# Optimization experiments

Hardware: AMD Instinct MI355X
Metric: run time of the kernel (lower is better)

## Reference

```python
import jax, jax.numpy as jnp
import numpy as np

L, H, FG, C = 2, 4, 8, 2            # n_layer, grid_heads, grid_feats, grid_channels
HNODE, HNET, HPIN = 96, 32, 16      # hidden node/net/pin feats
ONODE, ONET, NT = 32, 32, 4         # out node/net feats, n_target


def _leaky(x, s=0.01):
    return jnp.where(x >= 0, x, s * x)


def _edge_softmax(e, dst, n):
    # e: [E,H] scores, softmax over incoming edges per dst node
    m = jax.ops.segment_max(e, dst, num_segments=n)
    m = jnp.where(jnp.isfinite(m), m, 0.0)
    ex = jnp.exp(e - m[dst])
    s = jax.ops.segment_sum(ex, dst, num_segments=n)
    return ex / jnp.maximum(s[dst], 1e-9)


def _gat(x, src, dst, fc_w, attn_l, attn_r, bias, n):
    # DGL GATConv: fc (no bias), additive attention, leaky_relu(0.2), edge softmax, sum, +bias
    h = (x @ fc_w).reshape(n, H, FG)                      # [N,H,F]
    el = jnp.sum(h * attn_l, -1)                          # [N,H]
    er = jnp.sum(h * attn_r, -1)
    e = _leaky(el[src] + er[dst], 0.2)                    # [E,H]
    a = _edge_softmax(e, dst, n)
    out = jax.ops.segment_sum(h[src] * a[..., None], dst, num_segments=n)
    return out + bias.reshape(1, H, FG)                   # [N,H,F]


def _graphconv(x, src, dst, w, b, n_src, n_dst):
    # DGL GraphConv norm='both': D_src^-1/2 (xW) aggregated, D_dst^-1/2, + bias
    deg_out = jnp.maximum(jax.ops.segment_sum(jnp.ones(src.shape, jnp.float32), src, num_segments=n_src), 1.0)
    deg_in = jnp.maximum(jax.ops.segment_sum(jnp.ones(dst.shape, jnp.float32), dst, num_segments=n_dst), 1.0)
    h = (x * deg_out[:, None] ** -0.5) @ w
    agg = jax.ops.segment_sum(h[src], dst, num_segments=n_dst)
    return agg * deg_in[:, None] ** -0.5 + b


def _nnconv(x_src, src, dst, efeat, lin2_w, lin2_b, b, n_dst):
    # DGL NNConv (aggregator='mean'): per-edge weight matrix from edge_func=lin2
    W = (efeat @ lin2_w + lin2_b).reshape(-1, HNET, ONODE)   # [E,in,out]
    msg = jnp.einsum('ei,eio->eo', x_src[src], W)            # [E,out]
    deg = jnp.maximum(jax.ops.segment_sum(jnp.ones(dst.shape, jnp.float32), dst, num_segments=n_dst), 1.0)
    agg = jax.ops.segment_sum(msg, dst, num_segments=n_dst) / deg[:, None]
    return agg + b


def setup_inputs() -> dict:
    key = jax.random.key(0)
    ks = jax.random.split(key, 32)
    Nn, Nnet, Ep, Eg = 50000, 50000, 150000, 400000
    IN_NODE, IN_NET, IN_PIN = 16, 8, 8

    def rn(k, shape, scale=0.1):
        return jax.random.normal(k, shape, jnp.float32) * scale

    return {
        'in_node_feat': rn(ks[0], (Nn, IN_NODE), 1.0),
        'in_net_feat': rn(ks[1], (Nnet, IN_NET), 1.0),
        'in_pin_feat': rn(ks[2], (Ep, IN_PIN), 1.0),
        'node_lin_w': rn(ks[3], (IN_NODE, HNODE)), 'node_lin_b': rn(ks[4], (HNODE,)),
        'net_lin_w': rn(ks[5], (IN_NET, HNET)), 'net_lin_b': rn(ks[6], (HNET,)),
        'pin_lin_w': rn(ks[7], (IN_PIN, HPIN)), 'pin_lin_b': rn(ks[8], (HPIN,)),
        'gat_fc_w': rn(ks[9], (L, HNODE, H * FG)),
        'gat_attn_l': rn(ks[10], (L, H, FG)), 'gat_attn_r': rn(ks[11], (L, H, FG)),
        'gat_bias': rn(ks[12], (L, H * FG)),
        'gconv_w': rn(ks[13], (L, HNODE, ONET)), 'gconv_b': rn(ks[14], (L, ONET)),
        'lin2_w': rn(ks[15], (L, HPIN, HNET * ONODE)), 'lin2_b': rn(ks[16], (L, HNET * ONODE)),
        'nnconv_b': rn(ks[17], (L, ONODE)),
        'out1_w': rn(ks[18], (IN_NODE + HNODE, HNODE)), 'out1_b': rn(ks[19], (HNODE,)),
        'out2_w': rn(ks[20], (HNODE, HNODE)), 'out2_b': rn(ks[21], (HNODE,)),
        'out3_w': rn(ks[22], (HNODE, NT)), 'out3_b': rn(ks[23], (NT,)),
        'pins_src': jax.random.randint(ks[24], (Ep,), 0, Nn),
        'pins_dst': jax.random.randint(ks[25], (Ep,), 0, Nnet),
        'grid_src': jax.random.randint(ks[26], (C, Eg), 0, Nn),
        'grid_dst': jax.random.randint(ks[27], (C, Eg), 0, Nn),
    }


def reference(in_node_feat, in_net_feat, in_pin_feat, node_lin_w, node_lin_b,
              net_lin_w, net_lin_b, pin_lin_w, pin_lin_b, gat_fc_w, gat_attn_l,
              gat_attn_r, gat_bias, gconv_w, gconv_b, lin2_w, lin2_b, nnconv_b,
              out1_w, out1_b, out2_w, out2_b, out3_w, out3_b,
              pins_src, pins_dst, grid_src, grid_dst):
    Nn = in_node_feat.shape[0]
    Nnet = in_net_feat.shape[0]
    node = _leaky(in_node_feat @ node_lin_w + node_lin_b)
    net = _leaky(in_net_feat @ net_lin_w + net_lin_b)
    pin = _leaky(in_pin_feat @ pin_lin_w + pin_lin_b)
    for i in range(L):
        grids = [_gat(node, grid_src[j], grid_dst[j], gat_fc_w[i], gat_attn_l[i],
                      gat_attn_r[i], gat_bias[i], Nn) for j in range(C)]
        grid_out = jnp.concatenate(grids, -1).reshape(Nn, -1)   # [N, H*C*FG]
        # 'pins': node -> net (GraphConv); 'pinned': net -> node (NNConv, reversed pin edges)
        net_out = _graphconv(node, pins_src, pins_dst, gconv_w[i], gconv_b[i], Nn, Nnet)
        node_out = _nnconv(net, pins_dst, pins_src, pin, lin2_w[i], lin2_b[i], nnconv_b[i], Nn)
        node = jnp.tanh(jnp.concatenate([grid_out, node_out], -1))
        net = jnp.tanh(net_out)
    h = jnp.tanh(jnp.concatenate([in_node_feat, node], -1) @ out1_w + out1_b)
    h = jnp.tanh(h @ out2_w + out2_b)
    return jax.nn.sigmoid(h @ out3_w + out3_b)
```

## Files before the change

### kernel.cpp

```cpp
#include <hip/hip_runtime.h>
#include <math.h>


#define CAPG 48
#define CAPP 24
#define GB_U16 64
#define PD_U16 32
#define PS_STRIDE 64

typedef unsigned short ushort_t;
typedef unsigned int uint_t;
typedef __attribute__((ext_vector_type(8))) short bf16x8;
typedef __attribute__((ext_vector_type(4))) float f32x4;

static __device__ __forceinline__ float bf2f(ushort_t u) {
    return __uint_as_float(((unsigned)u) << 16);
}
static __device__ __forceinline__ ushort_t f2bf(float f) {
    unsigned i = __float_as_uint(f);
    unsigned r = (i + 0x7FFFu + ((i >> 16) & 1u)) >> 16;
    return (ushort_t)r;
}
static __device__ __forceinline__ uint_t pk2(float a, float b) {
    return (uint_t)f2bf(a) | ((uint_t)f2bf(b) << 16);
}
static __device__ __forceinline__ float lo2(uint_t u) { return __uint_as_float(u << 16); }
static __device__ __forceinline__ float hi2(uint_t u) { return __uint_as_float(u & 0xFFFF0000u); }

template <int ACT, int K1, int K2, int M, int R, bool OUT16>
__global__ void gemm_tiled(const float* __restrict__ X1,
                           const float* __restrict__ X2,
                           const float* __restrict__ rowscale,
                           const float* __restrict__ W,
                           const float* __restrict__ bias,
                           void* __restrict__ Yv, int N) {
    constexpr int K = K1 + K2;
    constexpr int MG = M / 4;
    constexpr int RG = 256 / MG;
    __shared__ float sW[K * M];
    for (int t = threadIdx.x; t < K * M; t += 256) sW[t] = W[t];
    __syncthreads();
    const float4* sW4 = (const float4*)sW;
    const int lane = threadIdx.x % MG;
    const int rsub = threadIdx.x / MG;
    if (rsub >= RG) return;
    const long long bstride = (long long)gridDim.x * RG * R;
    for (long long base = (long long)blockIdx.x * RG * R + rsub; base < N; base += bstride) {
        long long rows[R];
        bool ok[R];
        float4 acc[R];
#pragma unroll
        for (int j = 0; j < R; ++j) {
            rows[j] = base + (long long)j * RG;
            ok[j] = rows[j] < N;
            if (!ok[j]) rows[j] = base;
            acc[j] = {0.f, 0.f, 0.f, 0.f};
        }
        {
            const float4* x4[R];
#pragma unroll
            for (int j = 0; j < R; ++j) x4[j] = (const float4*)(X1 + rows[j] * K1);
#pragma unroll 2
            for (int k4 = 0; k4 < K1 / 4; ++k4) {
                float4 w0 = sW4[(k4 * 4 + 0) * MG + lane];
                float4 w1 = sW4[(k4 * 4 + 1) * MG + lane];
                float4 w2 = sW4[(k4 * 4 + 2) * MG + lane];
                float4 w3 = sW4[(k4 * 4 + 3) * MG + lane];
#pragma unroll
                for (int j = 0; j < R; ++j) {
                    float4 xv = x4[j][k4];
                    acc[j].x += xv.x * w0.x + xv.y * w1.x + xv.z * w2.x + xv.w * w3.x;
                    acc[j].y += xv.x * w0.y + xv.y * w1.y + xv.z * w2.y + xv.w * w3.y;
                    acc[j].z += xv.x * w0.z + xv.y * w1.z + xv.z * w2.z + xv.w * w3.z;
                    acc[j].w += xv.x * w0.w + xv.y * w1.w + xv.z * w2.w + xv.w * w3.w;
                }
            }
        }
        if (K2 > 0) {
            const float4* x4[R];
#pragma unroll
            for (int j = 0; j < R; ++j) x4[j] = (const float4*)(X2 + rows[j] * K2);
#pragma unroll 2
            for (int k4 = 0; k4 < K2 / 4; ++k4) {
                float4 w0 = sW4[(K1 + k4 * 4 + 0) * MG + lane];
                float4 w1 = sW4[(K1 + k4 * 4 + 1) * MG + lane];
                float4 w2 = sW4[(K1 + k4 * 4 + 2) * MG + lane];
                float4 w3 = sW4[(K1 + k4 * 4 + 3) * MG + lane];
#pragma unroll
                for (int j = 0; j < R; ++j) {
                    float4 xv = x4[j][k4];
                    acc[j].x += xv.x * w0.x + xv.y * w1.x + xv.z * w2.x + xv.w * w3.x;
                    acc[j].y += xv.x * w0.y + xv.y * w1.y + xv.z * w2.y + xv.w * w3.y;
                    acc[j].z += xv.x * w0.z + xv.y * w1.z + xv.z * w2.z + xv.w * w3.z;
                    acc[j].w += xv.x * w0.w + xv.y * w1.w + xv.z * w2.w + xv.w * w3.w;
                }
            }
        }
#pragma unroll
        for (int j = 0; j < R; ++j) {
            if (!ok[j]) continue;
            float4 a = acc[j];
            if (rowscale) {
                float rs = rowscale[rows[j]];
                a.x *= rs; a.y *= rs; a.z *= rs; a.w *= rs;
            }
            if (bias) {
                float4 bv = *(const float4*)(bias + lane * 4);
                a.x += bv.x; a.y += bv.y; a.z += bv.z; a.w += bv.w;
            }
            if (ACT == 1) {
                a.x = a.x >= 0.f ? a.x : 0.01f * a.x;
                a.y = a.y >= 0.f ? a.y : 0.01f * a.y;
                a.z = a.z >= 0.f ? a.z : 0.01f * a.z;
                a.w = a.w >= 0.f ? a.w : 0.01f * a.w;
            } else if (ACT == 2) {
                a.x = tanhf(a.x); a.y = tanhf(a.y);
                a.z = tanhf(a.z); a.w = tanhf(a.w);
            } else if (ACT == 3) {
                a.x = 1.f / (1.f + expf(-a.x)); a.y = 1.f / (1.f + expf(-a.y));
                a.z = 1.f / (1.f + expf(-a.z)); a.w = 1.f / (1.f + expf(-a.w));
            }
            if (OUT16) {
                uint2 v;
                v.x = pk2(a.x, a.y);
                v.y = pk2(a.z, a.w);
                *(uint2*)((ushort_t*)Yv + rows[j] * M + lane * 4) = v;
            } else {
                *(float4*)((float*)Yv + rows[j] * M + lane * 4) = a;
            }
        }
    }
}

__global__ void gemm_dual32(const float* __restrict__ X,
                            const float* __restrict__ rsN,
                            const float* __restrict__ W1,
                            const float* __restrict__ W2,
                            ushort_t* __restrict__ Y1, ushort_t* __restrict__ Y2, int N) {
    __shared__ float sW1[96 * 32];
    __shared__ float sW2[96 * 32];
    for (int t = threadIdx.x; t < 96 * 32; t += 256) {
        sW1[t] = W1[t];
        sW2[t] = W2[t];
    }
    __syncthreads();
    const float4* sW1_4 = (const float4*)sW1;
    const float4* sW2_4 = (const float4*)sW2;
    const int lane = threadIdx.x & 7;
    const int rsub = threadIdx.x >> 3;
    long long n0 = (long long)blockIdx.x * 64 + rsub;
    long long n1 = n0 + 32;
    if (n0 >= N) return;
    bool ok1 = n1 < N;
    const float4* x0 = (const float4*)(X + n0 * 96);
    const float4* x1 = (const float4*)(X + (ok1 ? n1 : n0) * 96);
    float4 a0 = {0.f, 0.f, 0.f, 0.f}, b0 = a0, a1 = a0, b1 = a0;
#pragma unroll 2
    for (int k4 = 0; k4 < 24; ++k4) {
        float4 xv0 = x0[k4];
        float4 xv1 = x1[k4];
#pragma unroll
        for (int kk = 0; kk < 4; ++kk) {
            float4 w1v = sW1_4[(k4 * 4 + kk) * 8 + lane];
            float4 w2v = sW2_4[(k4 * 4 + kk) * 8 + lane];
            float xs0 = kk == 0 ? xv0.x : kk == 1 ? xv0.y : kk == 2 ? xv0.z : xv0.w;
            float xs1 = kk == 0 ? xv1.x : kk == 1 ? xv1.y : kk == 2 ? xv1.z : xv1.w;
            a0.x += xs0 * w1v.x; a0.y += xs0 * w1v.y; a0.z += xs0 * w1v.z; a0.w += xs0 * w1v.w;
            b0.x += xs0 * w2v.x; b0.y += xs0 * w2v.y; b0.z += xs0 * w2v.z; b0.w += xs0 * w2v.w;
            a1.x += xs1 * w1v.x; a1.y += xs1 * w1v.y; a1.z += xs1 * w1v.z; a1.w += xs1 * w1v.w;
            b1.x += xs1 * w2v.x; b1.y += xs1 * w2v.y; b1.z += xs1 * w2v.z; b1.w += xs1 * w2v.w;
        }
    }
    {
        float rs = rsN[n0];
        uint2 va = {pk2(a0.x, a0.y), pk2(a0.z, a0.w)};
        uint2 vb = {pk2(b0.x * rs, b0.y * rs), pk2(b0.z * rs, b0.w * rs)};
        *(uint2*)(Y1 + n0 * 32 + lane * 4) = va;
        *(uint2*)(Y2 + n0 * 32 + lane * 4) = vb;
    }
    if (ok1) {
        float rs = rsN[n1];
        uint2 va = {pk2(a1.x, a1.y), pk2(a1.z, a1.w)};
        uint2 vb = {pk2(b1.x * rs, b1.y * rs), pk2(b1.z * rs, b1.w * rs)};
        *(uint2*)(Y1 + n1 * 32 + lane * 4) = va;
        *(uint2*)(Y2 + n1 * 32 + lane * 4) = vb;
    }
}

__global__ void zero_counts(ushort_t* __restrict__ gB0, ushort_t* __restrict__ gB1,
                            ushort_t* __restrict__ pdB, int* __restrict__ psB,
                            int Nn, int Nnet) {
    int i = blockIdx.x * blockDim.x + threadIdx.x;
    int mx = Nn > Nnet ? Nn : Nnet;
    for (; i < mx; i += gridDim.x * blockDim.x) {
        if (i < Nn) {
            *(int*)(gB0 + (long long)i * GB_U16) = 0;
            *(int*)(gB1 + (long long)i * GB_U16) = 0;
            psB[(long long)i * PS_STRIDE] = 0;
        }
        if (i < Nnet) *(int*)(pdB + (long long)i * PD_U16) = 0;
    }
}

__global__ void csr_build(const int* __restrict__ ps, const int* __restrict__ pd,
                          const int* __restrict__ gs0, const int* __restrict__ gd0,
                          const int* __restrict__ gs1, const int* __restrict__ gd1,
                          ushort_t* __restrict__ gB0, ushort_t* __restrict__ gB1,
                          ushort_t* __restrict__ pdB, int* __restrict__ psB,
                          int Ep, int Eg) {
    int total = 2 * Ep + 2 * Eg;
    for (int t = blockIdx.x * blockDim.x + threadIdx.x; t < total; t += gridDim.x * blockDim.x) {
        if (t < Ep) {
            int s = ps[t];
            int* b = psB + (long long)s * PS_STRIDE;
            int r = atomicAdd(b, 1);
            if (r < CAPP) ((int2*)b)[1 + r] = make_int2(t, pd[t]);
        } else if (t < 2 * Ep) {
            int e = t - Ep;
            int d = pd[e];
            ushort_t* b = pdB + (long long)d * PD_U16;
            int r = atomicAdd((int*)b, 1);
            if (r < CAPP) b[2 + r] = (ushort_t)ps[e];
        } else if (t < 2 * Ep + Eg) {
            int e = t - 2 * Ep;
            int d = gd0[e];
            ushort_t* b = gB0 + (long long)d * GB_U16;
            int r = atomicAdd((int*)b, 1);
            if (r < CAPG) b[2 + r] = (ushort_t)gs0[e];
        } else {
            int e = t - 2 * Ep - Eg;
            int d = gd1[e];
            ushort_t* b = gB1 + (long long)d * GB_U16;
            int r = atomicAdd((int*)b, 1);
            if (r < CAPG) b[2 + r] = (ushort_t)gs1[e];
        }
    }
}

__global__ void deg_xform2(const int* __restrict__ psB, const ushort_t* __restrict__ pdB,
                           float* __restrict__ rs, float* __restrict__ inv,
                           float* __restrict__ rsNet, int Nn, int Nnet) {
    int i = blockIdx.x * blockDim.x + threadIdx.x;
    int mx = Nn > Nnet ? Nn : Nnet;
    for (; i < mx; i += gridDim.x * blockDim.x) {
        if (i < Nn) {
            float d = fmaxf((float)psB[(long long)i * PS_STRIDE], 1.f);
            rs[i] = 1.f / sqrtf(d);
            inv[i] = 1.f / d;
        }
        if (i < Nnet) {
            float d = fmaxf((float)*(const int*)(pdB + (long long)i * PD_U16), 1.f);
            rsNet[i] = 1.f / sqrtf(d);
        }
    }
}

__global__ void gat_scores(const ushort_t* __restrict__ h, const float* __restrict__ al,
                           const float* __restrict__ ar, float* __restrict__ el,
                           float* __restrict__ er, int N) {
    int idx = blockIdx.x * blockDim.x + threadIdx.x;
    if (idx >= N * 4) return;
    int n = idx >> 2, hd = idx & 3;
    uint4 hv = *(const uint4*)(h + (long long)n * 32 + hd * 8);
    float f0 = lo2(hv.x), f1 = hi2(hv.x), f2 = lo2(hv.y), f3 = hi2(hv.y);
    float f4 = lo2(hv.z), f5 = hi2(hv.z), f6 = lo2(hv.w), f7 = hi2(hv.w);
    const float* a = al + hd * 8;
    const float* r = ar + hd * 8;
    float sl = f0 * a[0] + f1 * a[1] + f2 * a[2] + f3 * a[3] +
               f4 * a[4] + f5 * a[5] + f6 * a[6] + f7 * a[7];
    float sr = f0 * r[0] + f1 * r[1] + f2 * r[2] + f3 * r[3] +
               f4 * r[4] + f5 * r[5] + f6 * r[6] + f7 * r[7];
    el[idx] = sl;
    er[idx] = sr;
}

__global__ void gat_gather8(const ushort_t* __restrict__ gB0, const ushort_t* __restrict__ gB1,
                            const float* __restrict__ el, const float* __restrict__ er,
                            const ushort_t* __restrict__ gh, const float* __restrict__ gbias,
                            float* __restrict__ out, int N) {
    int idx = blockIdx.x * blockDim.x + threadIdx.x;
    if (idx >= N * 8) return;
    int d = idx >> 3;
    int rem = idx & 7;
    int hd = rem >> 1;
    int ch = rem & 1;
    float rd = er[d * 4 + hd];
    const ushort_t* b = (ch ? gB1 : gB0) + (long long)d * GB_U16;
    int c = *(const int*)b;
    c = c < CAPG ? c : CAPG;
    float sum = 0.f;
    float acc0 = 0.f, acc1 = 0.f, acc2 = 0.f, acc3 = 0.f;
    float acc4 = 0.f, acc5 = 0.f, acc6 = 0.f, acc7 = 0.f;
    for (int p = 0; p < c; ++p) {
        int s = b[2 + p];
        float v = el[s * 4 + hd] + rd;
        v = v >= 0.f ? v : 0.2f * v;
        float w = __expf(v);
        uint4 hv = *(const uint4*)(gh + (long long)s * 32 + hd * 8);
        sum += w;
        acc0 += w * lo2(hv.x); acc1 += w * hi2(hv.x);
        acc2 += w * lo2(hv.y); acc3 += w * hi2(hv.y);
        acc4 += w * lo2(hv.z); acc5 += w * hi2(hv.z);
        acc6 += w * lo2(hv.w); acc7 += w * hi2(hv.w);
    }
    float inv = 1.f / fmaxf(sum, 1e-9f);
    const float4* gb4 = (const float4*)(gbias + hd * 8);
    float4 b0 = gb4[0], b1 = gb4[1];
    float* op = out + (long long)d * 96 + hd * 16 + ch * 8;
    float4 r0, r1;
    r0.x = tanhf(acc0 * inv + b0.x); r0.y = tanhf(acc1 * inv + b0.y);
    r0.z = tanhf(acc2 * inv + b0.z); r0.w = tanhf(acc3 * inv + b0.w);
    r1.x = tanhf(acc4 * inv + b1.x); r1.y = tanhf(acc5 * inv + b1.y);
    r1.z = tanhf(acc6 * inv + b1.z); r1.w = tanhf(acc7 * inv + b1.w);
    *(float4*)(op) = r0;
    *(float4*)(op + 4) = r1;
}

__global__ void gconv_gather(const ushort_t* __restrict__ pdB, const ushort_t* __restrict__ h,
                             const float* __restrict__ rsNet, const float* __restrict__ gb,
                             ushort_t* __restrict__ out, int N) {
    long long total = (long long)N * 32;
    long long stride = (long long)gridDim.x * blockDim.x;
    for (long long idx = (long long)blockIdx.x * blockDim.x + threadIdx.x; idx < total; idx += stride) {
        int n = (int)(idx >> 5), c = (int)(idx & 31);
        const ushort_t* b = pdB + (long long)n * PD_U16;
        int cn = *(const int*)b;
        cn = cn < CAPP ? cn : CAPP;
        float acc = 0.f;
        for (int p = 0; p < cn; ++p) acc += bf2f(h[(long long)b[2 + p] * 32 + c]);
        out[idx] = f2bf(tanhf(acc * rsNet[n] + gb[c]));
    }
}

__global__ void nn_accum(const int* __restrict__ psB, const float* __restrict__ pinf,
                         const ushort_t* __restrict__ net, ushort_t* __restrict__ G, int N) {
    int t = blockIdx.x * blockDim.x + threadIdx.x;
    int n = t >> 5, i = t & 31;
    if (n >= N) return;
    const int* b = psB + (long long)n * PS_STRIDE;
    int cn = b[0]; cn = cn < CAPP ? cn : CAPP;
    const int2* ed2 = (const int2*)b + 1;
    float g[17];
#pragma unroll
    for (int k = 0; k < 17; ++k) g[k] = 0.f;
    for (int p = 0; p < cn; ++p) {
        int2 ed = ed2[p];
        float nv = bf2f(net[(long long)ed.y * 32 + i]);
        const float4* pr4 = (const float4*)(pinf + (long long)ed.x * 16);
        float4 a0 = pr4[0], a1 = pr4[1], a2 = pr4[2], a3 = pr4[3];
        g[0] += a0.x * nv;  g[1] += a0.y * nv;  g[2] += a0.z * nv;  g[3] += a0.w * nv;
        g[4] += a1.x * nv;  g[5] += a1.y * nv;  g[6] += a1.z * nv;  g[7] += a1.w * nv;
        g[8] += a2.x * nv;  g[9] += a2.y * nv;  g[10] += a2.z * nv; g[11] += a2.w * nv;
        g[12] += a3.x * nv; g[13] += a3.y * nv; g[14] += a3.z * nv; g[15] += a3.w * nv;
        g[16] += nv;
    }
    ushort_t* Gp = G + (long long)n * 544 + i;
#pragma unroll
    for (int k = 0; k < 17; ++k) Gp[k * 32] = f2bf(g[k]);
}

__launch_bounds__(256, 4)
__global__ void nn_gemm_mfma(const ushort_t* __restrict__ G,
                             const float* __restrict__ w,
                             const float* __restrict__ b2,
                             const float* __restrict__ invN,
                             const float* __restrict__ nnb,
                             float* __restrict__ out, int N) {
    __shared__ ushort_t sB[2 * 17 * 64 * 8];
    for (int idx = threadIdx.x; idx < 2 * 17 * 64 * 8; idx += 256) {
        int e = idx & 7;
        int l = (idx >> 3) & 63;
        int rest = idx >> 9;
        int s = rest % 17;
        int t = rest / 17;
        int grow = s * 32 + ((l >> 4) << 3) + e;
        int col = t * 16 + (l & 15);
        float v = (grow < 512) ? w[grow * 32 + col] : b2[(grow - 512) * 32 + col];
        sB[idx] = f2bf(v);
    }
    __syncthreads();
    const int lane = threadIdx.x & 63;
    const int wv = threadIdx.x >> 6;
    long long rowBase = (long long)blockIdx.x * 64 + (long long)wv * 16;
    if (rowBase >= N) return;
    const int r15 = lane & 15;
    const int kgrp = lane >> 4;
    long long arow = rowBase + r15;
    if (arow >= N) arow = N - 1;
    const ushort_t* gp = G + arow * 544 + kgrp * 8;
    f32x4 acc0 = {0.f, 0.f, 0.f, 0.f};
    f32x4 acc1 = {0.f, 0.f, 0.f, 0.f};
#pragma unroll
    for (int s = 0; s < 17; ++s) {
        bf16x8 a = *(const bf16x8*)(gp + s * 32);
        bf16x8 bb0 = *(const bf16x8*)(sB + ((0 * 17 + s) * 64 + lane) * 8);
        bf16x8 bb1 = *(const bf16x8*)(sB + ((1 * 17 + s) * 64 + lane) * 8);
        acc0 = __builtin_amdgcn_mfma_f32_16x16x32_bf16(a, bb0, acc0, 0, 0, 0);
        acc1 = __builtin_amdgcn_mfma_f32_16x16x32_bf16(a, bb1, acc1, 0, 0, 0);
    }
#pragma unroll
    for (int r = 0; r < 4; ++r) {
        long long row = rowBase + kgrp * 4 + r;
        if (row < N) {
            float iv = invN[row];
            float* op = out + row * 96 + 64;
            op[r15] = tanhf(acc0[r] * iv + nnb[r15]);
            op[16 + r15] = tanhf(acc1[r] * iv + nnb[16 + r15]);
        }
    }
}

__launch_bounds__(256, 4)
__global__ void mlp1_mfma(const float* __restrict__ X1, const float* __restrict__ X2,
                          const float* __restrict__ W, const float* __restrict__ bias,
                          ushort_t* __restrict__ Y, int N) {
    __shared__ ushort_t sB[6 * 4 * 64 * 8];
    for (int idx = threadIdx.x; idx < 6 * 4 * 64 * 8; idx += 256) {
        int e = idx & 7;
        int l = (idx >> 3) & 63;
        int rest = idx >> 9;
        int s = rest & 3;
        int t = rest >> 2;
        int grow = s * 32 + ((l >> 4) << 3) + e;
        int col = t * 16 + (l & 15);
        float v = (grow < 112) ? W[grow * 96 + col] : 0.f;
        sB[idx] = f2bf(v);
    }
    __syncthreads();
    const int lane = threadIdx.x & 63;
    const int wv = threadIdx.x >> 6;
    long long rowBase = (long long)blockIdx.x * 64 + (long long)wv * 16;
    if (rowBase >= N) return;
    const int r15 = lane & 15;
    const int kgrp = lane >> 4;
    long long arow = rowBase + r15;
    if (arow >= N) arow = N - 1;
    bf16x8 a[4];
#pragma unroll
    for (int s = 0; s < 4; ++s) {
        int k0 = s * 32 + kgrp * 8;
        float f[8];
        if (k0 < 16) {
            const float4* p = (const float4*)(X1 + arow * 16 + k0);
            float4 u = p[0], v = p[1];
            f[0] = u.x; f[1] = u.y; f[2] = u.z; f[3] = u.w;
            f[4] = v.x; f[5] = v.y; f[6] = v.z; f[7] = v.w;
        } else if (k0 < 112) {
            const float4* p = (const float4*)(X2 + arow * 96 + (k0 - 16));
            float4 u = p[0], v = p[1];
            f[0] = u.x; f[1] = u.y; f[2] = u.z; f[3] = u.w;
            f[4] = v.x; f[5] = v.y; f[6] = v.z; f[7] = v.w;
        } else {
#pragma unroll
            for (int j = 0; j < 8; ++j) f[j] = 0.f;
        }
        bf16x8 av;
#pragma unroll
        for (int j = 0; j < 8; ++j) av[j] = (short)f2bf(f[j]);
        a[s] = av;
    }
    f32x4 acc[6];
#pragma unroll
    for (int t = 0; t < 6; ++t) acc[t] = {0.f, 0.f, 0.f, 0.f};
#pragma unroll
    for (int s = 0; s < 4; ++s) {
#pragma unroll
        for (int t = 0; t < 6; ++t) {
            bf16x8 bb = *(const bf16x8*)(sB + ((t * 4 + s) * 64 + lane) * 8);
            acc[t] = __builtin_amdgcn_mfma_f32_16x16x32_bf16(a[s], bb, acc[t], 0, 0, 0);
        }
    }
#pragma unroll
    for (int r = 0; r < 4; ++r) {
        long long row = rowBase + kgrp * 4 + r;
        if (row < N) {
            ushort_t* op = Y + row * 96;
#pragma unroll
            for (int t = 0; t < 6; ++t) {
                int col = t * 16 + r15;
                op[col] = f2bf(tanhf(acc[t][r] + bias[col]));
            }
        }
    }
}

__launch_bounds__(256, 4)
__global__ void mlp2_mfma(const ushort_t* __restrict__ X,
                          const float* __restrict__ W, const float* __restrict__ bias,
                          float* __restrict__ Y, int N) {
    __shared__ ushort_t sB[6 * 3 * 64 * 8];
    for (int idx = threadIdx.x; idx < 6 * 3 * 64 * 8; idx += 256) {
        int e = idx & 7;
        int l = (idx >> 3) & 63;
        int rest = idx >> 9;
        int s = rest % 3;
        int t = rest / 3;
        int grow = s * 32 + ((l >> 4) << 3) + e;
        int col = t * 16 + (l & 15);
        sB[idx] = f2bf(W[grow * 96 + col]);
    }
    __syncthreads();
    const int lane = threadIdx.x & 63;
    const int wv = threadIdx.x >> 6;
    long long rowBase = (long long)blockIdx.x * 64 + (long long)wv * 16;
    if (rowBase >= N) return;
    const int r15 = lane & 15;
    const int kgrp = lane >> 4;
    long long arow = rowBase + r15;
    if (arow >= N) arow = N - 1;
    const ushort_t* xp = X + arow * 96 + kgrp * 8;
    f32x4 acc[6];
#pragma unroll
    for (int t = 0; t < 6; ++t) acc[t] = {0.f, 0.f, 0.f, 0.f};
#pragma unroll
    for (int s = 0; s < 3; ++s) {
        bf16x8 a = *(const bf16x8*)(xp + s * 32);
#pragma unroll
        for (int t = 0; t < 6; ++t) {
            bf16x8 bb = *(const bf16x8*)(sB + ((t * 3 + s) * 64 + lane) * 8);
            acc[t] = __builtin_amdgcn_mfma_f32_16x16x32_bf16(a, bb, acc[t], 0, 0, 0);
        }
    }
#pragma unroll
    for (int r = 0; r < 4; ++r) {
        long long row = rowBase + kgrp * 4 + r;
        if (row < N) {
            float* op = Y + row * 96;
#pragma unroll
            for (int t = 0; t < 6; ++t) {
                int col = t * 16 + r15;
                op[col] = tanhf(acc[t][r] + bias[col]);
            }
        }
    }
}

extern "C" void kernel_launch(void* const* d_in, const int* in_sizes, int n_in,
                              void* d_out, int out_size, void* d_ws, size_t ws_size,
                              hipStream_t stream) {
    const float* in_node = (const float*)d_in[0];
    const float* in_net = (const float*)d_in[1];
    const float* in_pinf = (const float*)d_in[2];
    const float* node_lin_w = (const float*)d_in[3];
    const float* node_lin_b = (const float*)d_in[4];
    const float* net_lin_w = (const float*)d_in[5];
    const float* net_lin_b = (const float*)d_in[6];
    const float* pin_lin_w = (const float*)d_in[7];
    const float* pin_lin_b = (const float*)d_in[8];
    const float* gat_fc_w = (const float*)d_in[9];
    const float* gat_attn_l = (const float*)d_in[10];
    const float* gat_attn_r = (const float*)d_in[11];
    const float* gat_bias = (const float*)d_in[12];
    const float* gconv_w = (const float*)d_in[13];
    const float* gconv_b = (const float*)d_in[14];
    const float* lin2_w = (const float*)d_in[15];
    const float* lin2_b = (const float*)d_in[16];
    const float* nnconv_bias = (const float*)d_in[17];
    const float* out1_w = (const float*)d_in[18];
    const float* out1_b = (const float*)d_in[19];
    const float* out2_w = (const float*)d_in[20];
    const float* out2_b = (const float*)d_in[21];
    const float* out3_w = (const float*)d_in[22];
    const float* out3_b = (const float*)d_in[23];
    const int* pins_src = (const int*)d_in[24];
    const int* pins_dst = (const int*)d_in[25];
    const int* grid_src = (const int*)d_in[26];
    const int* grid_dst = (const int*)d_in[27];

    const int Nn = in_sizes[0] / 16;
    const int Nnet = in_sizes[1] / 8;
    const int Ep = in_sizes[2] / 8;
    const int Eg = in_sizes[26] / 2;

    char* base = (char*)d_ws;
    size_t off = 0;
    auto alloc = [&](size_t bytes) -> void* {
        void* p = base + off;
        off += (bytes + 255) & ~(size_t)255;
        return p;
    };
    float* pin = (float*)alloc((size_t)Ep * 16 * 4);
    ushort_t* G = (ushort_t*)alloc((size_t)Nn * 544 * 2);
    float* rsN = (float*)alloc((size_t)Nn * 4);
    float* invN = (float*)alloc((size_t)Nn * 4);
    float* rsNet = (float*)alloc((size_t)Nnet * 4);
    ushort_t* gridB0 = (ushort_t*)alloc((size_t)Nn * GB_U16 * 2);
    ushort_t* gridB1 = (ushort_t*)alloc((size_t)Nn * GB_U16 * 2);
    ushort_t* pinDstB = (ushort_t*)alloc((size_t)Nnet * PD_U16 * 2);
    int* pinSrcB = (int*)alloc((size_t)Nn * PS_STRIDE * 4);
    float* nodeA = (float*)alloc((size_t)Nn * 96 * 4);
    float* nodeB = (float*)alloc((size_t)Nn * 96 * 4);
    ushort_t* netA = (ushort_t*)alloc((size_t)Nnet * 32 * 2);
    ushort_t* netB = (ushort_t*)alloc((size_t)Nnet * 32 * 2);
    ushort_t* gat_h = (ushort_t*)alloc((size_t)Nn * 32 * 2);
    float* el = (float*)alloc((size_t)Nn * 4 * 4);
    float* er = (float*)alloc((size_t)Nn * 4 * 4);
    ushort_t* gconv_h = (ushort_t*)alloc((size_t)Nn * 32 * 2);
    ushort_t* h1 = (ushort_t*)alloc((size_t)Nn * 96 * 2);

    auto gsz = [](long long total) -> int {
        long long b = (total + 255) / 256;
        if (b < 1) b = 1;
        if (b > 4096) b = 4096;
        return (int)b;
    };

    const int maxN = Nn > Nnet ? Nn : Nnet;
    const long long scatterT = 2LL * Ep + 2LL * Eg;

    zero_counts<<<gsz(maxN), 256, 0, stream>>>(gridB0, gridB1, pinDstB, pinSrcB, Nn, Nnet);
    csr_build<<<gsz(scatterT), 256, 0, stream>>>(pins_src, pins_dst,
                                                 grid_src, grid_dst, grid_src + Eg, grid_dst + Eg,
                                                 gridB0, gridB1, pinDstB, pinSrcB, Ep, Eg);
    deg_xform2<<<gsz(maxN), 256, 0, stream>>>(pinSrcB, pinDstB, rsN, invN, rsNet, Nn, Nnet);

    auto blocks_for = [](long long N, int M, int R) -> int {
        int rowsPerBlock = (256 / (M / 4)) * R;
        long long b = (N + rowsPerBlock - 1) / rowsPerBlock;
        if (b > 2048) b = 2048;
        if (b < 1) b = 1;
        return (int)b;
    };

    gemm_tiled<1, 16, 0, 96, 4, false><<<blocks_for(Nn, 96, 4), 256, 0, stream>>>(
        in_node, nullptr, nullptr, node_lin_w, node_lin_b, nodeA, Nn);
    gemm_tiled<1, 8, 0, 32, 2, true><<<blocks_for(Nnet, 32, 2), 256, 0, stream>>>(
        in_net, nullptr, nullptr, net_lin_w, net_lin_b, netA, Nnet);
    gemm_tiled<1, 8, 0, 16, 2, false><<<blocks_for(Ep, 16, 2), 256, 0, stream>>>(
        in_pinf, nullptr, nullptr, pin_lin_w, pin_lin_b, pin, Ep);

    float* node_cur = nodeA; float* node_nxt = nodeB;
    ushort_t* net_cur = netA; ushort_t* net_nxt = netB;

    for (int i = 0; i < 2; ++i) {
        gemm_dual32<<<(Nn + 63) / 64, 256, 0, stream>>>(
            node_cur, rsN, gat_fc_w + (size_t)i * 96 * 32, gconv_w + (size_t)i * 96 * 32,
            gat_h, gconv_h, Nn);
        gat_scores<<<(Nn * 4 + 255) / 256, 256, 0, stream>>>(
            gat_h, gat_attn_l + i * 32, gat_attn_r + i * 32, el, er, Nn);

        gat_gather8<<<(Nn * 8 + 255) / 256, 256, 0, stream>>>(
            gridB0, gridB1, el, er, gat_h, gat_bias + i * 32, node_nxt, Nn);

        gconv_gather<<<gsz((long long)Nnet * 32), 256, 0, stream>>>(
            pinDstB, gconv_h, rsNet, gconv_b + i * 32, net_nxt, Nnet);

        nn_accum<<<(Nn * 32 + 255) / 256, 256, 0, stream>>>(
            pinSrcB, pin, net_cur, G, Nn);
        nn_gemm_mfma<<<(Nn + 63) / 64, 256, 0, stream>>>(
            G, lin2_w + (size_t)i * 16 * 1024, lin2_b + (size_t)i * 1024,
            invN, nnconv_bias + i * 32, node_nxt, Nn);

        float* t = node_cur; node_cur = node_nxt; node_nxt = t;
        ushort_t* u = net_cur; net_cur = net_nxt; net_nxt = u;
    }

    mlp1_mfma<<<(Nn + 63) / 64, 256, 0, stream>>>(
        in_node, node_cur, out1_w, out1_b, h1, Nn);
    float* h2 = node_nxt;
    mlp2_mfma<<<(Nn + 63) / 64, 256, 0, stream>>>(
        h1, out2_w, out2_b, h2, Nn);
    gemm_tiled<3, 96, 0, 4, 1, false><<<blocks_for(Nn, 4, 1), 256, 0, stream>>>(
        h2, nullptr, nullptr, out3_w, out3_b, (float*)d_out, Nn);
}
```

Baseline: 345.6 us.

## Fuse NNConv edge accumulation with MFMA GEMM via shared memory; store pin feats bf16

Merges the per-node accumulation kernel and the MFMA GEMM into one kernel that builds the 16x544 G tile in LDS and multiplies it by lin2 weights there, so the large G intermediate never goes to global memory. Pin features are now stored as bf16, which halves their gather traffic. In exchange, each 512-thread block rebuilds the 17KB weight tile for only 16 rows, and only one wave does the MFMA while the other seven sit idle. LDS use per block also grows, which lowers occupancy.

```diff
diff --git a/kernel.cpp b/kernel.cpp
--- a/kernel.cpp
+++ b/kernel.cpp
@@ -332,42 +332,15 @@
     }
 }
 
-__global__ void nn_accum(const int* __restrict__ psB, const float* __restrict__ pinf,
-                         const ushort_t* __restrict__ net, ushort_t* __restrict__ G, int N) {
-    int t = blockIdx.x * blockDim.x + threadIdx.x;
-    int n = t >> 5, i = t & 31;
-    if (n >= N) return;
-    const int* b = psB + (long long)n * PS_STRIDE;
-    int cn = b[0]; cn = cn < CAPP ? cn : CAPP;
-    const int2* ed2 = (const int2*)b + 1;
-    float g[17];
-#pragma unroll
-    for (int k = 0; k < 17; ++k) g[k] = 0.f;
-    for (int p = 0; p < cn; ++p) {
-        int2 ed = ed2[p];
-        float nv = bf2f(net[(long long)ed.y * 32 + i]);
-        const float4* pr4 = (const float4*)(pinf + (long long)ed.x * 16);
-        float4 a0 = pr4[0], a1 = pr4[1], a2 = pr4[2], a3 = pr4[3];
-        g[0] += a0.x * nv;  g[1] += a0.y * nv;  g[2] += a0.z * nv;  g[3] += a0.w * nv;
-        g[4] += a1.x * nv;  g[5] += a1.y * nv;  g[6] += a1.z * nv;  g[7] += a1.w * nv;
-        g[8] += a2.x * nv;  g[9] += a2.y * nv;  g[10] += a2.z * nv; g[11] += a2.w * nv;
-        g[12] += a3.x * nv; g[13] += a3.y * nv; g[14] += a3.z * nv; g[15] += a3.w * nv;
-        g[16] += nv;
-    }
-    ushort_t* Gp = G + (long long)n * 544 + i;
-#pragma unroll
-    for (int k = 0; k < 17; ++k) Gp[k * 32] = f2bf(g[k]);
-}
-
-__launch_bounds__(256, 4)
-__global__ void nn_gemm_mfma(const ushort_t* __restrict__ G,
-                             const float* __restrict__ w,
-                             const float* __restrict__ b2,
-                             const float* __restrict__ invN,
-                             const float* __restrict__ nnb,
-                             float* __restrict__ out, int N) {
+__launch_bounds__(512, 1)
+__global__ void nn_fused(const int* __restrict__ psB, const ushort_t* __restrict__ pinf,
+                         const ushort_t* __restrict__ net,
+                         const float* __restrict__ w, const float* __restrict__ b2,
+                         const float* __restrict__ invN, const float* __restrict__ nnb,
+                         float* __restrict__ out, int N) {
+    __shared__ ushort_t sG[16 * 544];
     __shared__ ushort_t sB[2 * 17 * 64 * 8];
-    for (int idx = threadIdx.x; idx < 2 * 17 * 64 * 8; idx += 256) {
+    for (int idx = threadIdx.x; idx < 2 * 17 * 64 * 8; idx += 512) {
         int e = idx & 7;
         int l = (idx >> 3) & 63;
         int rest = idx >> 9;
@@ -378,34 +351,60 @@
         float v = (grow < 512) ? w[grow * 32 + col] : b2[(grow - 512) * 32 + col];
         sB[idx] = f2bf(v);
     }
+    const int n_local = threadIdx.x >> 5;
+    const int i = threadIdx.x & 31;
+    long long n = (long long)blockIdx.x * 16 + n_local;
+    float g[17];
+#pragma unroll
+    for (int k = 0; k < 17; ++k) g[k] = 0.f;
+    if (n < N) {
+        const int* b = psB + n * PS_STRIDE;
+        int cn = b[0]; cn = cn < CAPP ? cn : CAPP;
+        const int2* ed2 = (const int2*)b + 1;
+        for (int p = 0; p < cn; ++p) {
+            int2 ed = ed2[p];
+            float nv = bf2f(net[(long long)ed.y * 32 + i]);
+            const uint4* pr = (const uint4*)(pinf + (long long)ed.x * 16);
+            uint4 u0 = pr[0], u1 = pr[1];
+            g[0] += lo2(u0.x) * nv;  g[1] += hi2(u0.x) * nv;
+            g[2] += lo2(u0.y) * nv;  g[3] += hi2(u0.y) * nv;
+            g[4] += lo2(u0.z) * nv;  g[5] += hi2(u0.z) * nv;
+            g[6] += lo2(u0.w) * nv;  g[7] += hi2(u0.w) * nv;
+            g[8] += lo2(u1.x) * nv;  g[9] += hi2(u1.x) * nv;
+            g[10] += lo2(u1.y) * nv; g[11] += hi2(u1.y) * nv;
+            g[12] += lo2(u1.z) * nv; g[13] += hi2(u1.z) * nv;
+            g[14] += lo2(u1.w) * nv; g[15] += hi2(u1.w) * nv;
+            g[16] += nv;
+        }
+    }
+    ushort_t* gp = sG + n_local * 544 + i;
+#pragma unroll
+    for (int k = 0; k < 17; ++k) gp[k * 32] = f2bf(g[k]);
     __syncthreads();
-    const int lane = threadIdx.x & 63;
-    const int wv = threadIdx.x >> 6;
-    long long rowBase = (long long)blockIdx.x * 64 + (long long)wv * 16;
-    if (rowBase >= N) return;
-    const int r15 = lane & 15;
-    const int kgrp = lane >> 4;
-    long long arow = rowBase + r15;
-    if (arow >= N) arow = N - 1;
-    const ushort_t* gp = G + arow * 544 + kgrp * 8;
-    f32x4 acc0 = {0.f, 0.f, 0.f, 0.f};
-    f32x4 acc1 = {0.f, 0.f, 0.f, 0.f};
-#pragma unroll
-    for (int s = 0; s < 17; ++s) {
-        bf16x8 a = *(const bf16x8*)(gp + s * 32);
-        bf16x8 bb0 = *(const bf16x8*)(sB + ((0 * 17 + s) * 64 + lane) * 8);
-        bf16x8 bb1 = *(const bf16x8*)(sB + ((1 * 17 + s) * 64 + lane) * 8);
-        acc0 = __builtin_amdgcn_mfma_f32_16x16x32_bf16(a, bb0, acc0, 0, 0, 0);
-        acc1 = __builtin_amdgcn_mfma_f32_16x16x32_bf16(a, bb1, acc1, 0, 0, 0);
-    }
-#pragma unroll
-    for (int r = 0; r < 4; ++r) {
-        long long row = rowBase + kgrp * 4 + r;
-        if (row < N) {
-            float iv = invN[row];
-            float* op = out + row * 96 + 64;
-            op[r15] = tanhf(acc0[r] * iv + nnb[r15]);
-            op[16 + r15] = tanhf(acc1[r] * iv + nnb[16 + r15]);
+    if (threadIdx.x < 64) {
+        const int lane = threadIdx.x;
+        const int r15 = lane & 15;
+        const int kgrp = lane >> 4;
+        const ushort_t* ap = sG + r15 * 544 + kgrp * 8;
+        f32x4 acc0 = {0.f, 0.f, 0.f, 0.f};
+        f32x4 acc1 = {0.f, 0.f, 0.f, 0.f};
+#pragma unroll
+        for (int s = 0; s < 17; ++s) {
+            bf16x8 a = *(const bf16x8*)(ap + s * 32);
+            bf16x8 bb0 = *(const bf16x8*)(sB + ((0 * 17 + s) * 64 + lane) * 8);
+            bf16x8 bb1 = *(const bf16x8*)(sB + ((1 * 17 + s) * 64 + lane) * 8);
+            acc0 = __builtin_amdgcn_mfma_f32_16x16x32_bf16(a, bb0, acc0, 0, 0, 0);
+            acc1 = __builtin_amdgcn_mfma_f32_16x16x32_bf16(a, bb1, acc1, 0, 0, 0);
+        }
+#pragma unroll
+        for (int r = 0; r < 4; ++r) {
+            long long row = (long long)blockIdx.x * 16 + kgrp * 4 + r;
+            if (row < N) {
+                float iv = invN[row];
+                float* op = out + row * 96 + 64;
+                op[r15] = tanhf(acc0[r] * iv + nnb[r15]);
+                op[16 + r15] = tanhf(acc1[r] * iv + nnb[16 + r15]);
+            }
         }
     }
 }
@@ -579,8 +578,7 @@
         off += (bytes + 255) & ~(size_t)255;
         return p;
     };
-    float* pin = (float*)alloc((size_t)Ep * 16 * 4);
-    ushort_t* G = (ushort_t*)alloc((size_t)Nn * 544 * 2);
+    ushort_t* pin = (ushort_t*)alloc((size_t)Ep * 16 * 2);
     float* rsN = (float*)alloc((size_t)Nn * 4);
     float* invN = (float*)alloc((size_t)Nn * 4);
     float* rsNet = (float*)alloc((size_t)Nnet * 4);
@@ -626,7 +624,7 @@
         in_node, nullptr, nullptr, node_lin_w, node_lin_b, nodeA, Nn);
     gemm_tiled<1, 8, 0, 32, 2, true><<<blocks_for(Nnet, 32, 2), 256, 0, stream>>>(
         in_net, nullptr, nullptr, net_lin_w, net_lin_b, netA, Nnet);
-    gemm_tiled<1, 8, 0, 16, 2, false><<<blocks_for(Ep, 16, 2), 256, 0, stream>>>(
+    gemm_tiled<1, 8, 0, 16, 2, true><<<blocks_for(Ep, 16, 2), 256, 0, stream>>>(
         in_pinf, nullptr, nullptr, pin_lin_w, pin_lin_b, pin, Ep);
 
     float* node_cur = nodeA; float* node_nxt = nodeB;
@@ -645,11 +643,9 @@
         gconv_gather<<<gsz((long long)Nnet * 32), 256, 0, stream>>>(
             pinDstB, gconv_h, rsNet, gconv_b + i * 32, net_nxt, Nnet);
 
-        nn_accum<<<(Nn * 32 + 255) / 256, 256, 0, stream>>>(
-            pinSrcB, pin, net_cur, G, Nn);
-        nn_gemm_mfma<<<(Nn + 63) / 64, 256, 0, stream>>>(
-            G, lin2_w + (size_t)i * 16 * 1024, lin2_b + (size_t)i * 1024,
-            invN, nnconv_bias + i * 32, node_nxt, Nn);
+        nn_fused<<<(Nn + 15) / 16, 512, 0, stream>>>(
+            pinSrcB, pin, net_cur, lin2_w + (size_t)i * 16 * 1024,
+            lin2_b + (size_t)i * 1024, invN, nnconv_bias + i * 32, node_nxt, Nn);
 
         float* t = node_cur; node_cur = node_nxt; node_nxt = t;
         ushort_t* u = net_cur; net_cur = net_nxt; net_nxt = u;
```

Measured after the change: 404.8 us. 1.17x slower.
